# Kernel tuning notes

Measured on AMD Instinct MI355X. Metric: run time of the kernel, lower is better.

## Reference

```python
import jax, jax.numpy as jnp
import numpy as np

N = 50000
IN_DIM, HID_DIM, OUT_DIM = 16, 64, 32


def setup_inputs() -> dict:
    key = jax.random.key(0)
    k1, k2, k3, k4, k5 = jax.random.split(key, 5)
    x = jax.random.normal(k1, (N, IN_DIM), dtype=jnp.float32)
    edge_index = jax.random.randint(k2, (2, 800000), 0, N, dtype=jnp.int64)
    # GCNConv weights (glorot-ish scale) and biases
    W1 = jax.random.normal(k3, (IN_DIM, HID_DIM), dtype=jnp.float32) / np.sqrt(IN_DIM)
    b1 = jnp.zeros((HID_DIM,), dtype=jnp.float32)
    W2 = jax.random.normal(k4, (HID_DIM, OUT_DIM), dtype=jnp.float32) / np.sqrt(HID_DIM)
    b2 = jnpplus = jnp.zeros((OUT_DIM,), dtype=jnp.float32)
    return {"x": x, "edge_index": edge_index, "W1": W1, "b1": b1, "W2": W2, "b2": b2}


def _gcn_conv(x, src, dst, norm, W, b, num_nodes):
    # PyG GCNConv: h = X W; out[d] = sum_e norm_e * h[src_e]; out += b
    h = x @ W                                   # [N, D_out] small GEMM
    msgs = h[src] * norm[:, None]               # [E+N, D_out] gather (memory-bound)
    out = jax.ops.segment_sum(msgs, dst, num_segments=num_nodes)  # scatter-add
    return out + b


def reference(x, edge_index, W1, b1, W2, b2):
    num_nodes = x.shape[0]
    # add self-loops (PyG GCNConv default add_self_loops=True)
    loops = jnp.arange(num_nodes, dtype=edge_index.dtype)
    src = jnp.concatenate([edge_index[0], loops])
    dst = jnp.concatenate([edge_index[1], loops])
    # symmetric normalization D^{-1/2} (A+I) D^{-1/2}, degree over dst
    deg = jax.ops.segment_sum(jnp.ones_like(src, dtype=x.dtype), dst, num_segments=num_nodes)
    dinv = jnp.where(deg > 0, jax.lax.rsqrt(deg), 0.0)
    norm = dinv[src] * dinv[dst]                # [E+N]

    h = _gcn_conv(x, src, dst, norm, W1, b1, num_nodes)
    h = jax.nn.relu(h)
    out = _gcn_conv(h, src, dst, norm, W2, b2, num_nodes)
    return out
```

## Files before the change

kernel.cpp:

```cpp
#include <hip/hip_runtime.h>
#include <hip/hip_fp16.h>

#define IN_DIM  16
#define HID_DIM 64
#define OUT_DIM 32

#define CAP 8192
#define EPB 3328

__device__ __forceinline__ int detect_is64(const void* edges) {
    const int* w = (const int*)edges;
    int is64 = 1;
    #pragma unroll
    for (int i = 0; i < 16; ++i) is64 &= (w[2 * i + 1] == 0);
    return is64;
}

__device__ __forceinline__ long long edge_at(const void* edges, int is64, long long i) {
    if (is64) return ((const long long*)edges)[i];
    return (long long)((const int*)edges)[i];
}

__global__ __launch_bounds__(256) void k_partA(const void* edges, int* gcur,
                                               unsigned int* gpart, int nbuk, long long E) {
    __shared__ unsigned int staged[EPB];
    __shared__ int hcnt[256], hoff[256], hcur[256];
    __shared__ int s64s;
    int t = threadIdx.x;
    if (t == 0) s64s = detect_is64(edges);
    hcnt[t] = 0;
    __syncthreads();
    int is64 = s64s;

    long long e0 = (long long)blockIdx.x * EPB;
    unsigned int rs[13], rd[13];
    int nval = 0;
    #pragma unroll
    for (int k = 0; k < 13; ++k) {
        long long e = e0 + t + k * 256;
        if (e < E) {
            rs[k] = (unsigned int)edge_at(edges, is64, e);
            rd[k] = (unsigned int)edge_at(edges, is64, E + e);
            atomicAdd(&hcnt[rd[k] >> 8], 1);
            nval = k + 1;
        }
    }
    __syncthreads();

    int v = hcnt[t];
    hoff[t] = v;
    __syncthreads();
    for (int d = 1; d < 256; d <<= 1) {
        int u = (t >= d) ? hoff[t - d] : 0;
        __syncthreads();
        hoff[t] += u;
        __syncthreads();
    }
    int excl = hoff[t] - v;
    hoff[t] = excl;
    hcur[t] = excl;
    __syncthreads();

    #pragma unroll
    for (int k = 0; k < 13; ++k) {
        if (k < nval) {
            int p = atomicAdd(&hcur[rd[k] >> 8], 1);
            staged[p] = rs[k] | ((rd[k] & 255u) << 16);
        }
    }
    __syncthreads();

    if (t < nbuk) {
        int c = hcnt[t];
        if (c > 0) {
            int base = atomicAdd(&gcur[t], c);
            int o = hoff[t];
            for (int k = 0; k < c; ++k) {
                int idx = base + k;
                if (idx < CAP) gpart[(size_t)t * CAP + idx] = staged[o + k];
            }
        }
    }
}

__global__ __launch_bounds__(256) void k_partB(const int* __restrict__ gcur,
                                               const unsigned int* __restrict__ gpart,
                                               unsigned short* __restrict__ csr,
                                               int* __restrict__ offs,
                                               float* __restrict__ dinv,
                                               int nbuk, int N) {
    __shared__ unsigned int ebuf[CAP];
    __shared__ int bscan[256];
    __shared__ int hcnt[256], hoff[256], hcur[256];
    int t = threadIdx.x;
    int b = blockIdx.x;

    int bc = (t < nbuk) ? min(gcur[t], CAP) : 0;
    bscan[t] = bc;
    hcnt[t] = 0;
    __syncthreads();
    for (int d = 1; d < 256; d <<= 1) {
        int u = (t >= d) ? bscan[t - d] : 0;
        __syncthreads();
        bscan[t] += u;
        __syncthreads();
    }
    int base = (b == 0) ? 0 : bscan[b - 1];
    int cnt  = bscan[b] - base;

    for (int i = t; i < cnt; i += 256) ebuf[i] = gpart[(size_t)b * CAP + i];
    __syncthreads();
    for (int i = t; i < cnt; i += 256) atomicAdd(&hcnt[(ebuf[i] >> 16) & 255u], 1);
    __syncthreads();

    int v = hcnt[t];
    hoff[t] = v;
    __syncthreads();
    for (int d = 1; d < 256; d <<= 1) {
        int u = (t >= d) ? hoff[t - d] : 0;
        __syncthreads();
        hoff[t] += u;
        __syncthreads();
    }
    int excl = hoff[t] - v;
    hcur[t] = excl;
    __syncthreads();

    int node = b * 256 + t;
    if (node < N) {
        offs[node] = base + excl;
        dinv[node] = rsqrtf((float)v + 1.0f);
    }
    if (b == nbuk - 1 && t == 0) offs[N] = bscan[nbuk - 1];

    for (int i = t; i < cnt; i += 256) {
        unsigned int e = ebuf[i];
        int dl = (e >> 16) & 255;
        int p = atomicAdd(&hcur[dl], 1);
        csr[base + p] = (unsigned short)(e & 0xffffu);
    }
}

__global__ __launch_bounds__(256) void k_agg1(
    const float* __restrict__ x, const float* __restrict__ dinv,
    const int* __restrict__ offs, const unsigned short* __restrict__ csr,
    float* __restrict__ aggX, int N)
{
    int gtid = blockIdx.x * 256 + threadIdx.x;
    int lane = gtid & 63;
    int g = lane >> 4, sub = lane & 15;
    int comp = sub & 3, way = sub >> 2;
    int node = (gtid >> 6) * 4 + g;
    if (node >= N) return;
    const float4* x4 = (const float4*)x;
    float di = dinv[node];
    int start = offs[node], end = offs[node + 1];
    float4 acc = make_float4(0.f, 0.f, 0.f, 0.f);
    if (way == 0) {
        float4 xs = x4[(size_t)node * 4 + comp];
        acc = make_float4(di * xs.x, di * xs.y, di * xs.z, di * xs.w);
    }
    int j = start + way;
    for (; j + 4 < end; j += 8) {
        int s0 = csr[j], s1 = csr[j + 4];
        float w0 = dinv[s0], w1 = dinv[s1];
        float4 a0 = x4[(size_t)s0 * 4 + comp];
        float4 a1 = x4[(size_t)s1 * 4 + comp];
        acc.x += w0 * a0.x + w1 * a1.x; acc.y += w0 * a0.y + w1 * a1.y;
        acc.z += w0 * a0.z + w1 * a1.z; acc.w += w0 * a0.w + w1 * a1.w;
    }
    if (j < end) {
        int s = csr[j];
        float w = dinv[s];
        float4 a = x4[(size_t)s * 4 + comp];
        acc.x += w * a.x; acc.y += w * a.y; acc.z += w * a.z; acc.w += w * a.w;
    }
    #pragma unroll
    for (int m = 4; m <= 8; m <<= 1) {
        acc.x += __shfl_xor(acc.x, m, 64);
        acc.y += __shfl_xor(acc.y, m, 64);
        acc.z += __shfl_xor(acc.z, m, 64);
        acc.w += __shfl_xor(acc.w, m, 64);
    }
    if (way == 0)
        ((float4*)aggX)[(size_t)node * 4 + comp] =
            make_float4(di * acc.x, di * acc.y, di * acc.z, di * acc.w);
}

#define AGG_P 20
#define H1_P  68
__global__ __launch_bounds__(256) void k_gemm12(
    const float* __restrict__ aggX,
    const float* __restrict__ W1, const float* __restrict__ b1,
    const float* __restrict__ W2, __half* __restrict__ h2, int N)
{
    __shared__ float W1s[IN_DIM * HID_DIM];
    __shared__ float W2s[HID_DIM * OUT_DIM];
    __shared__ float b1s[HID_DIM];
    __shared__ float aggs[64 * AGG_P];
    __shared__ float h1s[64 * H1_P];

    int tid = threadIdx.x;
    int base = blockIdx.x * 64;
    for (int i = tid; i < IN_DIM * HID_DIM; i += 256) W1s[i] = W1[i];
    for (int i = tid; i < HID_DIM * OUT_DIM; i += 256) W2s[i] = W2[i];
    if (tid < HID_DIM) b1s[tid] = b1[tid];

    {
        int node = tid >> 2, comp = tid & 3;
        float4 v = (base + node < N) ? ((const float4*)aggX)[(size_t)(base + node) * 4 + comp]
                                     : make_float4(0.f, 0.f, 0.f, 0.f);
        *(float4*)&aggs[node * AGG_P + comp * 4] = v;
    }
    __syncthreads();

    int node = tid >> 2, q = tid & 3;

    {
        float acc[16];
        #pragma unroll
        for (int c = 0; c < 16; ++c) acc[c] = b1s[q * 16 + c];
        #pragma unroll
        for (int k = 0; k < IN_DIM; ++k) {
            float a = aggs[node * AGG_P + k];
            const float4* wr = (const float4*)&W1s[k * HID_DIM + q * 16];
            #pragma unroll
            for (int c4 = 0; c4 < 4; ++c4) {
                float4 w = wr[c4];
                acc[c4 * 4 + 0] += a * w.x; acc[c4 * 4 + 1] += a * w.y;
                acc[c4 * 4 + 2] += a * w.z; acc[c4 * 4 + 3] += a * w.w;
            }
        }
        float4* h1row = (float4*)&h1s[node * H1_P + q * 16];
        #pragma unroll
        for (int c4 = 0; c4 < 4; ++c4)
            h1row[c4] = make_float4(fmaxf(acc[c4 * 4 + 0], 0.f), fmaxf(acc[c4 * 4 + 1], 0.f),
                                    fmaxf(acc[c4 * 4 + 2], 0.f), fmaxf(acc[c4 * 4 + 3], 0.f));
    }
    __syncthreads();

    {
        float acc2[8];
        #pragma unroll
        for (int c = 0; c < 8; ++c) acc2[c] = 0.f;
        const float4* h1row = (const float4*)&h1s[node * H1_P];
        #pragma unroll
        for (int k4 = 0; k4 < 16; ++k4) {
            float4 hv = h1row[k4];
            float hvv[4] = {hv.x, hv.y, hv.z, hv.w};
            #pragma unroll
            for (int kk = 0; kk < 4; ++kk) {
                int k = k4 * 4 + kk;
                const float4* wr = (const float4*)&W2s[k * OUT_DIM + q * 8];
                float4 w0 = wr[0], w1 = wr[1];
                acc2[0] += hvv[kk] * w0.x; acc2[1] += hvv[kk] * w0.y;
                acc2[2] += hvv[kk] * w0.z; acc2[3] += hvv[kk] * w0.w;
                acc2[4] += hvv[kk] * w1.x; acc2[5] += hvv[kk] * w1.y;
                acc2[6] += hvv[kk] * w1.z; acc2[7] += hvv[kk] * w1.w;
            }
        }
        if (base + node < N) {
            __half2 p[4];
            #pragma unroll
            for (int c = 0; c < 4; ++c)
                p[c] = __floats2half2_rn(acc2[c * 2], acc2[c * 2 + 1]);
            ((uint4*)h2)[(size_t)(base + node) * 4 + q] = *(uint4*)p;
        }
    }
}

__global__ __launch_bounds__(256) void k_agg2(
    const __half* __restrict__ h2, const float* __restrict__ dinv,
    const int* __restrict__ offs, const unsigned short* __restrict__ csr,
    const float* __restrict__ b2, float* __restrict__ out, int N)
{
    int gtid = blockIdx.x * 256 + threadIdx.x;
    int lane = gtid & 63;
    int g = lane >> 4, sub = lane & 15;
    int comp = sub & 3, way = sub >> 2;
    int node = (gtid >> 6) * 4 + g;
    if (node >= N) return;
    const uint4* h24 = (const uint4*)h2;
    float di = dinv[node];
    int start = offs[node], end = offs[node + 1];
    float acc[8] = {0.f, 0.f, 0.f, 0.f, 0.f, 0.f, 0.f, 0.f};
    if (way == 0) {
        uint4 r = h24[(size_t)node * 4 + comp];
        const __half2* hp = (const __half2*)&r;
        #pragma unroll
        for (int c = 0; c < 4; ++c) {
            float2 f = __half22float2(hp[c]);
            acc[c * 2]     = di * f.x;
            acc[c * 2 + 1] = di * f.y;
        }
    }
    int j = start + way;
    for (; j + 4 < end; j += 8) {
        int s0 = csr[j], s1 = csr[j + 4];
        float w0 = dinv[s0], w1 = dinv[s1];
        uint4 r0 = h24[(size_t)s0 * 4 + comp];
        uint4 r1 = h24[(size_t)s1 * 4 + comp];
        const __half2* hp0 = (const __half2*)&r0;
        const __half2* hp1 = (const __half2*)&r1;
        #pragma unroll
        for (int c = 0; c < 4; ++c) {
            float2 f0 = __half22float2(hp0[c]);
            float2 f1 = __half22float2(hp1[c]);
            acc[c * 2]     += w0 * f0.x + w1 * f1.x;
            acc[c * 2 + 1] += w0 * f0.y + w1 * f1.y;
        }
    }
    if (j < end) {
        int s = csr[j];
        float w = dinv[s];
        uint4 r = h24[(size_t)s * 4 + comp];
        const __half2* hp = (const __half2*)&r;
        #pragma unroll
        for (int c = 0; c < 4; ++c) {
            float2 f = __half22float2(hp[c]);
            acc[c * 2]     += w * f.x;
            acc[c * 2 + 1] += w * f.y;
        }
    }
    #pragma unroll
    for (int m = 4; m <= 8; m <<= 1) {
        #pragma unroll
        for (int c = 0; c < 8; ++c) acc[c] += __shfl_xor(acc[c], m, 64);
    }
    if (way == 0) {
        const float4* b24 = (const float4*)b2;
        float4 bb0 = b24[comp * 2], bb1 = b24[comp * 2 + 1];
        float4* out4 = (float4*)out;
        out4[(size_t)node * 8 + comp * 2 + 0] =
            make_float4(di * acc[0] + bb0.x, di * acc[1] + bb0.y,
                        di * acc[2] + bb0.z, di * acc[3] + bb0.w);
        out4[(size_t)node * 8 + comp * 2 + 1] =
            make_float4(di * acc[4] + bb1.x, di * acc[5] + bb1.y,
                        di * acc[6] + bb1.z, di * acc[7] + bb1.w);
    }
}

extern "C" void kernel_launch(void* const* d_in, const int* in_sizes, int n_in,
                              void* d_out, int out_size, void* d_ws, size_t ws_size,
                              hipStream_t stream) {
    const float* x     = (const float*)d_in[0];
    const void*  edges = d_in[1];
    const float* W1    = (const float*)d_in[2];
    const float* b1    = (const float*)d_in[3];
    const float* W2    = (const float*)d_in[4];
    const float* b2    = (const float*)d_in[5];
    float* out = (float*)d_out;

    const int       N = in_sizes[0] / IN_DIM;
    const long long E = in_sizes[1] / 2;
    const int    NBUK = (N + 255) >> 8;

    unsigned short* csr   = (unsigned short*)d_ws;
    unsigned int*   gpart = (unsigned int*)(csr + ((E + 7) & ~7LL));
    float*  aggX     = (float*)(gpart + (size_t)NBUK * CAP);
    __half* h2       = (__half*)(aggX + (size_t)IN_DIM * N);
    float*  dinv     = (float*)(h2 + (size_t)OUT_DIM * N);
    int*    offs     = (int*)(dinv + N);
    int*    gcur     = offs + N + 1;

    const int B = 256;
    hipMemsetAsync(gcur, 0, (size_t)NBUK * sizeof(int), stream);
    k_partA<<<(int)((E + EPB - 1) / EPB), B, 0, stream>>>(edges, gcur, gpart, NBUK, E);
    k_partB<<<NBUK, B, 0, stream>>>(gcur, gpart, csr, offs, dinv, NBUK, N);

    k_agg1<<<(N + 15) / 16, B, 0, stream>>>(x, dinv, offs, csr, aggX, N);
    k_gemm12<<<(N + 63) / 64, B, 0, stream>>>(aggX, W1, b1, W2, h2, N);
    k_agg2<<<(N + 15) / 16, B, 0, stream>>>(h2, dinv, offs, csr, b2, out, N);
}
```

Before: 137.5 us.

## Fuse layer-1 aggregation with both GEMMs and parallelize partition write-out

Merges the first-layer neighbor aggregation kernel into the dense GEMM kernel, so aggregated features stay in shared memory instead of making a global round trip, and one launch is removed. Each block now handles 16 nodes, with only one wave doing the GEMMs after aggregation, and each block reloads the weight matrices. Separately, the partition kernel's bucket scatter is spread across all four waves with lanes writing contiguous slots, replacing one serial thread per bucket. The fused GEMM leaves 3 of 4 waves idle and repeats the weight loads in 4x more blocks. It also swaps a barrier for a waitcnt, which is only safe because the one active wave writes and reads its own rows of h1s.

New measurement: 139.8 us. About the same (+1.7%).

```diff
diff --git a/kernel.cpp b/kernel.cpp
--- a/kernel.cpp
+++ b/kernel.cpp
@@ -24,7 +24,7 @@
 __global__ __launch_bounds__(256) void k_partA(const void* edges, int* gcur,
                                                unsigned int* gpart, int nbuk, long long E) {
     __shared__ unsigned int staged[EPB];
-    __shared__ int hcnt[256], hoff[256], hcur[256];
+    __shared__ int hcnt[256], hoff[256], hcur[256], hbase[256];
     __shared__ int s64s;
     int t = threadIdx.x;
     if (t == 0) s64s = detect_is64(edges);
@@ -68,17 +68,18 @@
             staged[p] = rs[k] | ((rd[k] & 255u) << 16);
         }
     }
-    __syncthreads();
-
     if (t < nbuk) {
         int c = hcnt[t];
-        if (c > 0) {
-            int base = atomicAdd(&gcur[t], c);
-            int o = hoff[t];
-            for (int k = 0; k < c; ++k) {
-                int idx = base + k;
-                if (idx < CAP) gpart[(size_t)t * CAP + idx] = staged[o + k];
-            }
+        hbase[t] = (c > 0) ? atomicAdd(&gcur[t], c) : 0;
+    }
+    __syncthreads();
+
+    int wid = t >> 6, lane = t & 63;
+    for (int b = wid; b < nbuk; b += 4) {
+        int c = hcnt[b], o = hoff[b], base = hbase[b];
+        for (int oo = lane; oo < c; oo += 64) {
+            int idx = base + oo;
+            if (idx < CAP) gpart[(size_t)b * CAP + idx] = staged[o + oo];
         }
     }
 }
@@ -141,80 +142,71 @@
     }
 }
 
-__global__ __launch_bounds__(256) void k_agg1(
+#define AGG_P 20
+#define H1_P  68
+__global__ __launch_bounds__(256) void k_agg1gemm(
     const float* __restrict__ x, const float* __restrict__ dinv,
     const int* __restrict__ offs, const unsigned short* __restrict__ csr,
-    float* __restrict__ aggX, int N)
-{
-    int gtid = blockIdx.x * 256 + threadIdx.x;
-    int lane = gtid & 63;
-    int g = lane >> 4, sub = lane & 15;
-    int comp = sub & 3, way = sub >> 2;
-    int node = (gtid >> 6) * 4 + g;
-    if (node >= N) return;
-    const float4* x4 = (const float4*)x;
-    float di = dinv[node];
-    int start = offs[node], end = offs[node + 1];
-    float4 acc = make_float4(0.f, 0.f, 0.f, 0.f);
-    if (way == 0) {
-        float4 xs = x4[(size_t)node * 4 + comp];
-        acc = make_float4(di * xs.x, di * xs.y, di * xs.z, di * xs.w);
-    }
-    int j = start + way;
-    for (; j + 4 < end; j += 8) {
-        int s0 = csr[j], s1 = csr[j + 4];
-        float w0 = dinv[s0], w1 = dinv[s1];
-        float4 a0 = x4[(size_t)s0 * 4 + comp];
-        float4 a1 = x4[(size_t)s1 * 4 + comp];
-        acc.x += w0 * a0.x + w1 * a1.x; acc.y += w0 * a0.y + w1 * a1.y;
-        acc.z += w0 * a0.z + w1 * a1.z; acc.w += w0 * a0.w + w1 * a1.w;
-    }
-    if (j < end) {
-        int s = csr[j];
-        float w = dinv[s];
-        float4 a = x4[(size_t)s * 4 + comp];
-        acc.x += w * a.x; acc.y += w * a.y; acc.z += w * a.z; acc.w += w * a.w;
-    }
-    #pragma unroll
-    for (int m = 4; m <= 8; m <<= 1) {
-        acc.x += __shfl_xor(acc.x, m, 64);
-        acc.y += __shfl_xor(acc.y, m, 64);
-        acc.z += __shfl_xor(acc.z, m, 64);
-        acc.w += __shfl_xor(acc.w, m, 64);
-    }
-    if (way == 0)
-        ((float4*)aggX)[(size_t)node * 4 + comp] =
-            make_float4(di * acc.x, di * acc.y, di * acc.z, di * acc.w);
-}
-
-#define AGG_P 20
-#define H1_P  68
-__global__ __launch_bounds__(256) void k_gemm12(
-    const float* __restrict__ aggX,
     const float* __restrict__ W1, const float* __restrict__ b1,
     const float* __restrict__ W2, __half* __restrict__ h2, int N)
 {
     __shared__ float W1s[IN_DIM * HID_DIM];
     __shared__ float W2s[HID_DIM * OUT_DIM];
     __shared__ float b1s[HID_DIM];
-    __shared__ float aggs[64 * AGG_P];
-    __shared__ float h1s[64 * H1_P];
+    __shared__ float aggs[16 * AGG_P];
+    __shared__ float h1s[16 * H1_P];
 
     int tid = threadIdx.x;
-    int base = blockIdx.x * 64;
+    int nbase = blockIdx.x * 16;
     for (int i = tid; i < IN_DIM * HID_DIM; i += 256) W1s[i] = W1[i];
     for (int i = tid; i < HID_DIM * OUT_DIM; i += 256) W2s[i] = W2[i];
     if (tid < HID_DIM) b1s[tid] = b1[tid];
 
-    {
-        int node = tid >> 2, comp = tid & 3;
-        float4 v = (base + node < N) ? ((const float4*)aggX)[(size_t)(base + node) * 4 + comp]
-                                     : make_float4(0.f, 0.f, 0.f, 0.f);
-        *(float4*)&aggs[node * AGG_P + comp * 4] = v;
-    }
-    __syncthreads();
-
-    int node = tid >> 2, q = tid & 3;
+    int lane = tid & 63;
+    int g = lane >> 4, sub = lane & 15;
+    int comp = sub & 3, way = sub >> 2;
+    int nl = (tid >> 6) * 4 + g;
+    int node = nbase + nl;
+    if (node < N) {
+        const float4* x4 = (const float4*)x;
+        float di = dinv[node];
+        int start = offs[node], end = offs[node + 1];
+        float4 acc = make_float4(0.f, 0.f, 0.f, 0.f);
+        if (way == 0) {
+            float4 xs = x4[(size_t)node * 4 + comp];
+            acc = make_float4(di * xs.x, di * xs.y, di * xs.z, di * xs.w);
+        }
+        int j = start + way;
+        for (; j + 4 < end; j += 8) {
+            int s0 = csr[j], s1 = csr[j + 4];
+            float w0 = dinv[s0], w1 = dinv[s1];
+            float4 a0 = x4[(size_t)s0 * 4 + comp];
+            float4 a1 = x4[(size_t)s1 * 4 + comp];
+            acc.x += w0 * a0.x + w1 * a1.x; acc.y += w0 * a0.y + w1 * a1.y;
+            acc.z += w0 * a0.z + w1 * a1.z; acc.w += w0 * a0.w + w1 * a1.w;
+        }
+        if (j < end) {
+            int s = csr[j];
+            float w = dinv[s];
+            float4 a = x4[(size_t)s * 4 + comp];
+            acc.x += w * a.x; acc.y += w * a.y; acc.z += w * a.z; acc.w += w * a.w;
+        }
+        #pragma unroll
+        for (int m = 4; m <= 8; m <<= 1) {
+            acc.x += __shfl_xor(acc.x, m, 64);
+            acc.y += __shfl_xor(acc.y, m, 64);
+            acc.z += __shfl_xor(acc.z, m, 64);
+            acc.w += __shfl_xor(acc.w, m, 64);
+        }
+        if (way == 0)
+            *(float4*)&aggs[nl * AGG_P + comp * 4] =
+                make_float4(di * acc.x, di * acc.y, di * acc.z, di * acc.w);
+    }
+    __syncthreads();
+
+    if (tid >= 64) return;
+    int n2 = tid >> 2, q = tid & 3;
+    int gnode = nbase + n2;
 
     {
         float acc[16];
@@ -222,7 +214,7 @@
         for (int c = 0; c < 16; ++c) acc[c] = b1s[q * 16 + c];
         #pragma unroll
         for (int k = 0; k < IN_DIM; ++k) {
-            float a = aggs[node * AGG_P + k];
+            float a = aggs[n2 * AGG_P + k];
             const float4* wr = (const float4*)&W1s[k * HID_DIM + q * 16];
             #pragma unroll
             for (int c4 = 0; c4 < 4; ++c4) {
@@ -231,19 +223,19 @@
                 acc[c4 * 4 + 2] += a * w.z; acc[c4 * 4 + 3] += a * w.w;
             }
         }
-        float4* h1row = (float4*)&h1s[node * H1_P + q * 16];
+        float4* h1row = (float4*)&h1s[n2 * H1_P + q * 16];
         #pragma unroll
         for (int c4 = 0; c4 < 4; ++c4)
             h1row[c4] = make_float4(fmaxf(acc[c4 * 4 + 0], 0.f), fmaxf(acc[c4 * 4 + 1], 0.f),
                                     fmaxf(acc[c4 * 4 + 2], 0.f), fmaxf(acc[c4 * 4 + 3], 0.f));
     }
-    __syncthreads();
+    __builtin_amdgcn_s_waitcnt(0);
 
     {
         float acc2[8];
         #pragma unroll
         for (int c = 0; c < 8; ++c) acc2[c] = 0.f;
-        const float4* h1row = (const float4*)&h1s[node * H1_P];
+        const float4* h1row = (const float4*)&h1s[n2 * H1_P];
         #pragma unroll
         for (int k4 = 0; k4 < 16; ++k4) {
             float4 hv = h1row[k4];
@@ -259,12 +251,12 @@
                 acc2[6] += hvv[kk] * w1.z; acc2[7] += hvv[kk] * w1.w;
             }
         }
-        if (base + node < N) {
+        if (gnode < N) {
             __half2 p[4];
             #pragma unroll
             for (int c = 0; c < 4; ++c)
                 p[c] = __floats2half2_rn(acc2[c * 2], acc2[c * 2 + 1]);
-            ((uint4*)h2)[(size_t)(base + node) * 4 + q] = *(uint4*)p;
+            ((uint4*)h2)[(size_t)gnode * 4 + q] = *(uint4*)p;
         }
     }
 }
@@ -357,8 +349,7 @@
 
     unsigned short* csr   = (unsigned short*)d_ws;
     unsigned int*   gpart = (unsigned int*)(csr + ((E + 7) & ~7LL));
-    float*  aggX     = (float*)(gpart + (size_t)NBUK * CAP);
-    __half* h2       = (__half*)(aggX + (size_t)IN_DIM * N);
+    __half* h2       = (__half*)(gpart + (size_t)NBUK * CAP);
     float*  dinv     = (float*)(h2 + (size_t)OUT_DIM * N);
     int*    offs     = (int*)(dinv + N);
     int*    gcur     = offs + N + 1;
@@ -368,7 +359,6 @@
     k_partA<<<(int)((E + EPB - 1) / EPB), B, 0, stream>>>(edges, gcur, gpart, NBUK, E);
     k_partB<<<NBUK, B, 0, stream>>>(gcur, gpart, csr, offs, dinv, NBUK, N);
 
-    k_agg1<<<(N + 15) / 16, B, 0, stream>>>(x, dinv, offs, csr, aggX, N);
-    k_gemm12<<<(N + 63) / 64, B, 0, stream>>>(aggX, W1, b1, W2, h2, N);
+    k_agg1gemm<<<(N + 15) / 16, B, 0, stream>>>(x, dinv, offs, csr, W1, b1, W2, h2, N);
     k_agg2<<<(N + 15) / 16, B, 0, stream>>>(h2, dinv, offs, csr, b2, out, N);
 }
```
